# Kernel tuning notes

Hardware: AMD Instinct MI355X
Metric: run time of the kernel (lower is better)

The kernel has to match this reference:

```python
import jax, jax.numpy as jnp
import numpy as np

N = 1_000_000   # gaussians
K_NB = 10       # neighbor control points per gaussian
K_TOTAL = 300   # num_fine control points


def _normalize(q, eps=1e-8):
    return q / jnp.maximum(jnp.linalg.norm(q, axis=-1, keepdims=True), eps)


def quaternion_to_rotation_matrix(q):
    # q: [..., 4] in (w, x, y, z); normalized before conversion
    q = _normalize(q)
    w, x, y, z = q[..., 0], q[..., 1], q[..., 2], q[..., 3]
    R = jnp.stack([
        jnp.stack([1 - 2 * (y * y + z * z), 2 * (x * y - w * z), 2 * (x * z + w * y)], axis=-1),
        jnp.stack([2 * (x * y + w * z), 1 - 2 * (x * x + z * z), 2 * (y * z - w * x)], axis=-1),
        jnp.stack([2 * (x * z - w * y), 2 * (y * z + w * x), 1 - 2 * (x * x + y * y)], axis=-1),
    ], axis=-2)  # [..., 3, 3]
    return R


def quaternion_multiply(a, b):
    # Hamilton product, (w, x, y, z)
    aw, ax, ay, az = a[..., 0], a[..., 1], a[..., 2], a[..., 3]
    bw, bx, by, bz = b[..., 0], b[..., 1], b[..., 2], b[..., 3]
    return jnp.stack([
        aw * bw - ax * bx - ay * by - az * bz,
        aw * bx + ax * bw + ay * bz - az * by,
        aw * by - ax * bz + ay * bw + az * bx,
        aw * bz + ax * by - ay * bx + az * bw,
    ], axis=-1)


def setup_inputs() -> dict:
    key = jax.random.key(0)
    ks = jax.random.split(key, 7)
    means = jax.random.normal(ks[0], (N, 3), dtype=jnp.float32)
    quaternions = _normalize(jax.random.normal(ks[1], (N, 4), dtype=jnp.float32))
    w = jax.random.uniform(ks[2], (N, K_NB), dtype=jnp.float32) + 1e-3
    weights = w / w.sum(-1, keepdims=True)  # blending weights sum to 1
    indices = jax.random.randint(ks[3], (N, K_NB), 0, K_TOTAL)
    ctrl_translations = 0.1 * jax.random.normal(ks[4], (K_TOTAL, 3), dtype=jnp.float32)
    ctrl_rotations = _normalize(jax.random.normal(ks[5], (K_TOTAL, 4), dtype=jnp.float32))
    ctrl_positions = jax.random.normal(ks[6], (K_TOTAL, 3), dtype=jnp.float32)
    return {
        'means': means, 'quaternions': quaternions, 'weights': weights,
        'ctrl_translations': ctrl_translations, 'ctrl_rotations': ctrl_rotations,
        'ctrl_positions': ctrl_positions, 'indices': indices,
    }


def reference(means, quaternions, weights, ctrl_translations, ctrl_rotations, ctrl_positions, indices):
    # gather neighbor control-point transforms
    nb_trans = ctrl_translations[indices]   # [N, K, 3]
    nb_rots = ctrl_rotations[indices]       # [N, K, 4]
    nb_pos = ctrl_positions[indices]        # [N, K, 3]

    diff = means[:, None, :] - nb_pos                       # [N, K, 3]
    R_ctrl = quaternion_to_rotation_matrix(nb_rots)         # [N, K, 3, 3]
    rotated_diff = jnp.einsum('nkij,nkj->nki', R_ctrl, diff)
    deformed_per_cp = rotated_diff + nb_pos + nb_trans      # [N, K, 3]

    w = weights[..., None]                                  # [N, K, 1]
    deformed_means = (w * deformed_per_cp).sum(axis=1)      # [N, 3]

    blended_rot = _normalize((w * nb_rots).sum(axis=1))     # [N, 4]
    deformed_quats = quaternion_multiply(blended_rot, quaternions)
    return deformed_means, deformed_quats
```

## Files before the change

kernel.cpp:

```cpp
#include <hip/hip_runtime.h>
#include <math.h>


__device__ __forceinline__ void compute_cp(
    const float* __restrict__ ctrl_trans,
    const float* __restrict__ ctrl_rot,
    const float* __restrict__ ctrl_pos,
    int cp, float4* q_out, float4* b_out)
{
    float qw = ctrl_rot[cp * 4 + 0];
    float qx = ctrl_rot[cp * 4 + 1];
    float qy = ctrl_rot[cp * 4 + 2];
    float qz = ctrl_rot[cp * 4 + 3];
    float n   = sqrtf(qw * qw + qx * qx + qy * qy + qz * qz);
    float inv = 1.0f / fmaxf(n, 1e-8f);
    float w = qw * inv, x = qx * inv, y = qy * inv, z = qz * inv;
    float R00 = 1.0f - 2.0f * (y * y + z * z);
    float R01 = 2.0f * (x * y - w * z);
    float R02 = 2.0f * (x * z + w * y);
    float R10 = 2.0f * (x * y + w * z);
    float R11 = 1.0f - 2.0f * (x * x + z * z);
    float R12 = 2.0f * (y * z - w * x);
    float R20 = 2.0f * (x * z - w * y);
    float R21 = 2.0f * (y * z + w * x);
    float R22 = 1.0f - 2.0f * (x * x + y * y);
    float px = ctrl_pos[cp * 3 + 0];
    float py = ctrl_pos[cp * 3 + 1];
    float pz = ctrl_pos[cp * 3 + 2];
    float tx = ctrl_trans[cp * 3 + 0];
    float ty = ctrl_trans[cp * 3 + 1];
    float tz = ctrl_trans[cp * 3 + 2];
    *q_out = make_float4(w, x, y, z);
    *b_out = make_float4(px + tx - (R00 * px + R01 * py + R02 * pz),
                         py + ty - (R10 * px + R11 * py + R12 * pz),
                         pz + tz - (R20 * px + R21 * py + R22 * pz),
                         0.0f);
}

struct Accum {
    float W;
    float Mxx, Myy, Mzz, Mxy, Mxz, Myz, Mwx, Mwy, Mwz;
    float qsw, qsx, qsy, qsz;
    float bsx, bsy, bsz;
};

__device__ __forceinline__ void acc_init(Accum& a) {
    a.W = 0.0f;
    a.Mxx = a.Myy = a.Mzz = 0.0f;
    a.Mxy = a.Mxz = a.Myz = 0.0f;
    a.Mwx = a.Mwy = a.Mwz = 0.0f;
    a.qsw = a.qsx = a.qsy = a.qsz = 0.0f;
    a.bsx = a.bsy = a.bsz = 0.0f;
}

__device__ __forceinline__ void acc_neighbor(Accum& a, const float4* __restrict__ s4,
                                             int cp, float w) {
    float4 q = s4[2 * cp];
    float4 b = s4[2 * cp + 1];
    float tw = w * q.x, tx = w * q.y, ty = w * q.z, tz = w * q.w;
    a.W += w;
    a.Mxx = fmaf(tx, q.y, a.Mxx);
    a.Myy = fmaf(ty, q.z, a.Myy);
    a.Mzz = fmaf(tz, q.w, a.Mzz);
    a.Mxy = fmaf(tx, q.z, a.Mxy);
    a.Mxz = fmaf(tx, q.w, a.Mxz);
    a.Myz = fmaf(ty, q.w, a.Myz);
    a.Mwx = fmaf(tw, q.y, a.Mwx);
    a.Mwy = fmaf(tw, q.z, a.Mwy);
    a.Mwz = fmaf(tw, q.w, a.Mwz);
    a.qsw += tw; a.qsx += tx; a.qsy += ty; a.qsz += tz;
    a.bsx = fmaf(w, b.x, a.bsx);
    a.bsy = fmaf(w, b.y, a.bsy);
    a.bsz = fmaf(w, b.z, a.bsz);
}

__device__ __forceinline__ void acc_epilogue(const Accum& a,
                                             float mx, float my, float mz,
                                             float4 g,
                                             float* dmx, float* dmy, float* dmz,
                                             float4* oq) {
    float A00 = a.W - 2.0f * (a.Myy + a.Mzz);
    float A01 = 2.0f * (a.Mxy - a.Mwz);
    float A02 = 2.0f * (a.Mxz + a.Mwy);
    float A10 = 2.0f * (a.Mxy + a.Mwz);
    float A11 = a.W - 2.0f * (a.Mxx + a.Mzz);
    float A12 = 2.0f * (a.Myz - a.Mwx);
    float A20 = 2.0f * (a.Mxz - a.Mwy);
    float A21 = 2.0f * (a.Myz + a.Mwx);
    float A22 = a.W - 2.0f * (a.Mxx + a.Myy);

    *dmx = fmaf(A00, mx, fmaf(A01, my, fmaf(A02, mz, a.bsx)));
    *dmy = fmaf(A10, mx, fmaf(A11, my, fmaf(A12, mz, a.bsy)));
    *dmz = fmaf(A20, mx, fmaf(A21, my, fmaf(A22, mz, a.bsz)));

    float n   = sqrtf(a.qsw * a.qsw + a.qsx * a.qsx + a.qsy * a.qsy + a.qsz * a.qsz);
    float inv = 1.0f / fmaxf(n, 1e-8f);
    float bw = a.qsw * inv, bx = a.qsx * inv, by = a.qsy * inv, bz = a.qsz * inv;

    float gw = g.x, gx = g.y, gy = g.z, gz = g.w;
    oq->x = bw * gw - bx * gx - by * gy - bz * gz;
    oq->y = bw * gx + bx * gw + by * gz - bz * gy;
    oq->z = bw * gy - bx * gz + by * gw + bz * gx;
    oq->w = bw * gz + bx * gy - by * gx + bz * gw;
}

__global__ __launch_bounds__(256) void deform_pair_kernel(
    const float* __restrict__ means,
    const float* __restrict__ quats,
    const float* __restrict__ weights,
    const float* __restrict__ ctrl_trans,
    const float* __restrict__ ctrl_rot,
    const float* __restrict__ ctrl_pos,
    const int*   __restrict__ indices,
    float* __restrict__ out_means,
    float* __restrict__ out_quats,
    int N, int K_TOTAL)
{
    extern __shared__ float4 s4[];
    for (int cp = threadIdx.x; cp < K_TOTAL; cp += blockDim.x) {
        float4 q, b;
        compute_cp(ctrl_trans, ctrl_rot, ctrl_pos, cp, &q, &b);
        s4[2 * cp]     = q;
        s4[2 * cp + 1] = b;
    }
    __syncthreads();

    long long tid = (long long)blockIdx.x * blockDim.x + threadIdx.x;
    long long i0  = 2 * tid;
    if (i0 >= N) return;

    if (i0 + 1 < N) {
        const int4*   ip = (const int4*)(indices + i0 * 10);
        const float4* wp = (const float4*)(weights + i0 * 10);
        int4   I0 = ip[0], I1 = ip[1], I2 = ip[2], I3 = ip[3], I4 = ip[4];
        float4 W0 = wp[0], W1 = wp[1], W2 = wp[2], W3 = wp[3], W4 = wp[4];

        Accum a0; acc_init(a0);
        acc_neighbor(a0, s4, I0.x, W0.x);
        acc_neighbor(a0, s4, I0.y, W0.y);
        acc_neighbor(a0, s4, I0.z, W0.z);
        acc_neighbor(a0, s4, I0.w, W0.w);
        acc_neighbor(a0, s4, I1.x, W1.x);
        acc_neighbor(a0, s4, I1.y, W1.y);
        acc_neighbor(a0, s4, I1.z, W1.z);
        acc_neighbor(a0, s4, I1.w, W1.w);
        acc_neighbor(a0, s4, I2.x, W2.x);
        acc_neighbor(a0, s4, I2.y, W2.y);

        Accum a1; acc_init(a1);
        acc_neighbor(a1, s4, I2.z, W2.z);
        acc_neighbor(a1, s4, I2.w, W2.w);
        acc_neighbor(a1, s4, I3.x, W3.x);
        acc_neighbor(a1, s4, I3.y, W3.y);
        acc_neighbor(a1, s4, I3.z, W3.z);
        acc_neighbor(a1, s4, I3.w, W3.w);
        acc_neighbor(a1, s4, I4.x, W4.x);
        acc_neighbor(a1, s4, I4.y, W4.y);
        acc_neighbor(a1, s4, I4.z, W4.z);
        acc_neighbor(a1, s4, I4.w, W4.w);

        const float2* mp = (const float2*)(means + i0 * 3);
        float2 m01 = mp[0], m23 = mp[1], m45 = mp[2];

        float4 g0 = ((const float4*)quats)[i0];
        float4 g1 = ((const float4*)quats)[i0 + 1];

        float d0x, d0y, d0z, d1x, d1y, d1z;
        float4 oq0, oq1;
        acc_epilogue(a0, m01.x, m01.y, m23.x, g0, &d0x, &d0y, &d0z, &oq0);
        acc_epilogue(a1, m23.y, m45.x, m45.y, g1, &d1x, &d1y, &d1z, &oq1);

        float2* omp = (float2*)(out_means + i0 * 3);
        omp[0] = make_float2(d0x, d0y);
        omp[1] = make_float2(d0z, d1x);
        omp[2] = make_float2(d1y, d1z);

        float4* oqp = (float4*)(out_quats + i0 * 4);
        oqp[0] = oq0;
        oqp[1] = oq1;
    } else {
        const int*   idx_row = indices + i0 * 10;
        const float* w_row   = weights + i0 * 10;
        Accum a0; acc_init(a0);
#pragma unroll
        for (int k = 0; k < 10; k++)
            acc_neighbor(a0, s4, idx_row[k], w_row[k]);

        float mx = means[i0 * 3 + 0];
        float my = means[i0 * 3 + 1];
        float mz = means[i0 * 3 + 2];
        float4 g0 = ((const float4*)quats)[i0];
        float dx, dy, dz;
        float4 oq0;
        acc_epilogue(a0, mx, my, mz, g0, &dx, &dy, &dz, &oq0);
        out_means[i0 * 3 + 0] = dx;
        out_means[i0 * 3 + 1] = dy;
        out_means[i0 * 3 + 2] = dz;
        ((float4*)out_quats)[i0] = oq0;
    }
}

__global__ __launch_bounds__(256) void deform_generic_kernel(
    const float* __restrict__ means,
    const float* __restrict__ quats,
    const float* __restrict__ weights,
    const float* __restrict__ ctrl_trans,
    const float* __restrict__ ctrl_rot,
    const float* __restrict__ ctrl_pos,
    const int*   __restrict__ indices,
    float* __restrict__ out_means,
    float* __restrict__ out_quats,
    int N, int K_NB, int K_TOTAL)
{
    extern __shared__ float4 s4[];
    for (int cp = threadIdx.x; cp < K_TOTAL; cp += blockDim.x) {
        float4 q, b;
        compute_cp(ctrl_trans, ctrl_rot, ctrl_pos, cp, &q, &b);
        s4[2 * cp]     = q;
        s4[2 * cp + 1] = b;
    }
    __syncthreads();

    long long i = (long long)blockIdx.x * blockDim.x + threadIdx.x;
    if (i >= N) return;

    const int*   idx_row = indices + i * K_NB;
    const float* w_row   = weights + i * K_NB;
    Accum a0; acc_init(a0);
    for (int k = 0; k < K_NB; k++)
        acc_neighbor(a0, s4, idx_row[k], w_row[k]);

    float mx = means[i * 3 + 0];
    float my = means[i * 3 + 1];
    float mz = means[i * 3 + 2];
    float4 g0 = ((const float4*)quats)[i];
    float dx, dy, dz;
    float4 oq0;
    acc_epilogue(a0, mx, my, mz, g0, &dx, &dy, &dz, &oq0);
    out_means[i * 3 + 0] = dx;
    out_means[i * 3 + 1] = dy;
    out_means[i * 3 + 2] = dz;
    ((float4*)out_quats)[i] = oq0;
}

extern "C" void kernel_launch(void* const* d_in, const int* in_sizes, int n_in,
                              void* d_out, int out_size, void* d_ws, size_t ws_size,
                              hipStream_t stream) {
    const float* means      = (const float*)d_in[0];
    const float* quats      = (const float*)d_in[1];
    const float* weights    = (const float*)d_in[2];
    const float* ctrl_trans = (const float*)d_in[3];
    const float* ctrl_rot   = (const float*)d_in[4];
    const float* ctrl_pos   = (const float*)d_in[5];
    const int*   indices    = (const int*)d_in[6];

    int N       = in_sizes[0] / 3;
    int K_NB    = in_sizes[2] / N;
    int K_TOTAL = in_sizes[3] / 3;

    float* out_means = (float*)d_out;
    float* out_quats = (float*)d_out + (long long)N * 3;

    int block = 256;
    size_t smem = (size_t)K_TOTAL * 2 * sizeof(float4);

    if (K_NB == 10) {
        long long pairs = ((long long)N + 1) / 2;
        int grid = (int)((pairs + block - 1) / block);
        deform_pair_kernel<<<grid, block, smem, stream>>>(
            means, quats, weights, ctrl_trans, ctrl_rot, ctrl_pos, indices,
            out_means, out_quats, N, K_TOTAL);
    } else {
        int grid = (int)(((long long)N + block - 1) / block);
        deform_generic_kernel<<<grid, block, smem, stream>>>(
            means, quats, weights, ctrl_trans, ctrl_rot, ctrl_pos, indices,
            out_means, out_quats, N, K_NB, K_TOTAL);
    }
}
```

Before: 149.4 us.

## Use grid-stride persistent blocks and split shared control-point table into SoA

The pair kernel now launches at most 1536 blocks that loop over pairs with a grid stride. Each block therefore builds the control-point table in shared memory once and reuses it for many pairs, instead of every one of roughly 2000 blocks recomputing it. The shared table moves from interleaved (q, b) pairs to two separate arrays, which changes the LDS bank access pattern. Loads of means and quats are also hoisted ahead of the accumulation, and ctrl_rot is read as a single float4. The risk is that fewer resident blocks per CU reduce the memory-level parallelism available to hide latency.

```diff
diff --git a/kernel.cpp b/kernel.cpp
--- a/kernel.cpp
+++ b/kernel.cpp
@@ -8,10 +8,8 @@
     const float* __restrict__ ctrl_pos,
     int cp, float4* q_out, float4* b_out)
 {
-    float qw = ctrl_rot[cp * 4 + 0];
-    float qx = ctrl_rot[cp * 4 + 1];
-    float qy = ctrl_rot[cp * 4 + 2];
-    float qz = ctrl_rot[cp * 4 + 3];
+    float4 qv = ((const float4*)ctrl_rot)[cp];
+    float qw = qv.x, qx = qv.y, qy = qv.z, qz = qv.w;
     float n   = sqrtf(qw * qw + qx * qx + qy * qy + qz * qz);
     float inv = 1.0f / fmaxf(n, 1e-8f);
     float w = qw * inv, x = qx * inv, y = qy * inv, z = qz * inv;
@@ -54,9 +52,9 @@
 }
 
 __device__ __forceinline__ void acc_neighbor(Accum& a, const float4* __restrict__ s4,
-                                             int cp, float w) {
-    float4 q = s4[2 * cp];
-    float4 b = s4[2 * cp + 1];
+                                             int K_TOTAL, int cp, float w) {
+    float4 q = s4[cp];
+    float4 b = s4[K_TOTAL + cp];
     float tw = w * q.x, tx = w * q.y, ty = w * q.z, tz = w * q.w;
     a.W += w;
     a.Mxx = fmaf(tx, q.y, a.Mxx);
@@ -114,89 +112,89 @@
     const int*   __restrict__ indices,
     float* __restrict__ out_means,
     float* __restrict__ out_quats,
-    int N, int K_TOTAL)
+    int N, int K_TOTAL, long long n_pairs)
 {
     extern __shared__ float4 s4[];
     for (int cp = threadIdx.x; cp < K_TOTAL; cp += blockDim.x) {
         float4 q, b;
         compute_cp(ctrl_trans, ctrl_rot, ctrl_pos, cp, &q, &b);
-        s4[2 * cp]     = q;
-        s4[2 * cp + 1] = b;
+        s4[cp]           = q;
+        s4[K_TOTAL + cp] = b;
     }
     __syncthreads();
 
-    long long tid = (long long)blockIdx.x * blockDim.x + threadIdx.x;
-    long long i0  = 2 * tid;
-    if (i0 >= N) return;
-
-    if (i0 + 1 < N) {
-        const int4*   ip = (const int4*)(indices + i0 * 10);
-        const float4* wp = (const float4*)(weights + i0 * 10);
-        int4   I0 = ip[0], I1 = ip[1], I2 = ip[2], I3 = ip[3], I4 = ip[4];
-        float4 W0 = wp[0], W1 = wp[1], W2 = wp[2], W3 = wp[3], W4 = wp[4];
-
-        Accum a0; acc_init(a0);
-        acc_neighbor(a0, s4, I0.x, W0.x);
-        acc_neighbor(a0, s4, I0.y, W0.y);
-        acc_neighbor(a0, s4, I0.z, W0.z);
-        acc_neighbor(a0, s4, I0.w, W0.w);
-        acc_neighbor(a0, s4, I1.x, W1.x);
-        acc_neighbor(a0, s4, I1.y, W1.y);
-        acc_neighbor(a0, s4, I1.z, W1.z);
-        acc_neighbor(a0, s4, I1.w, W1.w);
-        acc_neighbor(a0, s4, I2.x, W2.x);
-        acc_neighbor(a0, s4, I2.y, W2.y);
-
-        Accum a1; acc_init(a1);
-        acc_neighbor(a1, s4, I2.z, W2.z);
-        acc_neighbor(a1, s4, I2.w, W2.w);
-        acc_neighbor(a1, s4, I3.x, W3.x);
-        acc_neighbor(a1, s4, I3.y, W3.y);
-        acc_neighbor(a1, s4, I3.z, W3.z);
-        acc_neighbor(a1, s4, I3.w, W3.w);
-        acc_neighbor(a1, s4, I4.x, W4.x);
-        acc_neighbor(a1, s4, I4.y, W4.y);
-        acc_neighbor(a1, s4, I4.z, W4.z);
-        acc_neighbor(a1, s4, I4.w, W4.w);
-
-        const float2* mp = (const float2*)(means + i0 * 3);
-        float2 m01 = mp[0], m23 = mp[1], m45 = mp[2];
-
-        float4 g0 = ((const float4*)quats)[i0];
-        float4 g1 = ((const float4*)quats)[i0 + 1];
-
-        float d0x, d0y, d0z, d1x, d1y, d1z;
-        float4 oq0, oq1;
-        acc_epilogue(a0, m01.x, m01.y, m23.x, g0, &d0x, &d0y, &d0z, &oq0);
-        acc_epilogue(a1, m23.y, m45.x, m45.y, g1, &d1x, &d1y, &d1z, &oq1);
-
-        float2* omp = (float2*)(out_means + i0 * 3);
-        omp[0] = make_float2(d0x, d0y);
-        omp[1] = make_float2(d0z, d1x);
-        omp[2] = make_float2(d1y, d1z);
-
-        float4* oqp = (float4*)(out_quats + i0 * 4);
-        oqp[0] = oq0;
-        oqp[1] = oq1;
-    } else {
-        const int*   idx_row = indices + i0 * 10;
-        const float* w_row   = weights + i0 * 10;
-        Accum a0; acc_init(a0);
+    long long stride = (long long)gridDim.x * blockDim.x;
+    for (long long p = (long long)blockIdx.x * blockDim.x + threadIdx.x;
+         p < n_pairs; p += stride) {
+        long long i0 = 2 * p;
+
+        if (i0 + 1 < N) {
+            const int4*   ip = (const int4*)(indices + i0 * 10);
+            const float4* wp = (const float4*)(weights + i0 * 10);
+            int4   I0 = ip[0], I1 = ip[1], I2 = ip[2], I3 = ip[3], I4 = ip[4];
+            float4 W0 = wp[0], W1 = wp[1], W2 = wp[2], W3 = wp[3], W4 = wp[4];
+            const float2* mp = (const float2*)(means + i0 * 3);
+            float2 m01 = mp[0], m23 = mp[1], m45 = mp[2];
+            float4 g0 = ((const float4*)quats)[i0];
+            float4 g1 = ((const float4*)quats)[i0 + 1];
+
+            Accum a0; acc_init(a0);
+            acc_neighbor(a0, s4, K_TOTAL, I0.x, W0.x);
+            acc_neighbor(a0, s4, K_TOTAL, I0.y, W0.y);
+            acc_neighbor(a0, s4, K_TOTAL, I0.z, W0.z);
+            acc_neighbor(a0, s4, K_TOTAL, I0.w, W0.w);
+            acc_neighbor(a0, s4, K_TOTAL, I1.x, W1.x);
+            acc_neighbor(a0, s4, K_TOTAL, I1.y, W1.y);
+            acc_neighbor(a0, s4, K_TOTAL, I1.z, W1.z);
+            acc_neighbor(a0, s4, K_TOTAL, I1.w, W1.w);
+            acc_neighbor(a0, s4, K_TOTAL, I2.x, W2.x);
+            acc_neighbor(a0, s4, K_TOTAL, I2.y, W2.y);
+
+            Accum a1; acc_init(a1);
+            acc_neighbor(a1, s4, K_TOTAL, I2.z, W2.z);
+            acc_neighbor(a1, s4, K_TOTAL, I2.w, W2.w);
+            acc_neighbor(a1, s4, K_TOTAL, I3.x, W3.x);
+            acc_neighbor(a1, s4, K_TOTAL, I3.y, W3.y);
+            acc_neighbor(a1, s4, K_TOTAL, I3.z, W3.z);
+            acc_neighbor(a1, s4, K_TOTAL, I3.w, W3.w);
+            acc_neighbor(a1, s4, K_TOTAL, I4.x, W4.x);
+            acc_neighbor(a1, s4, K_TOTAL, I4.y, W4.y);
+            acc_neighbor(a1, s4, K_TOTAL, I4.z, W4.z);
+            acc_neighbor(a1, s4, K_TOTAL, I4.w, W4.w);
+
+            float d0x, d0y, d0z, d1x, d1y, d1z;
+            float4 oq0, oq1;
+            acc_epilogue(a0, m01.x, m01.y, m23.x, g0, &d0x, &d0y, &d0z, &oq0);
+            acc_epilogue(a1, m23.y, m45.x, m45.y, g1, &d1x, &d1y, &d1z, &oq1);
+
+            float2* omp = (float2*)(out_means + i0 * 3);
+            omp[0] = make_float2(d0x, d0y);
+            omp[1] = make_float2(d0z, d1x);
+            omp[2] = make_float2(d1y, d1z);
+
+            float4* oqp = (float4*)(out_quats + i0 * 4);
+            oqp[0] = oq0;
+            oqp[1] = oq1;
+        } else {
+            const int*   idx_row = indices + i0 * 10;
+            const float* w_row   = weights + i0 * 10;
+            Accum a0; acc_init(a0);
 #pragma unroll
-        for (int k = 0; k < 10; k++)
-            acc_neighbor(a0, s4, idx_row[k], w_row[k]);
-
-        float mx = means[i0 * 3 + 0];
-        float my = means[i0 * 3 + 1];
-        float mz = means[i0 * 3 + 2];
-        float4 g0 = ((const float4*)quats)[i0];
-        float dx, dy, dz;
-        float4 oq0;
-        acc_epilogue(a0, mx, my, mz, g0, &dx, &dy, &dz, &oq0);
-        out_means[i0 * 3 + 0] = dx;
-        out_means[i0 * 3 + 1] = dy;
-        out_means[i0 * 3 + 2] = dz;
-        ((float4*)out_quats)[i0] = oq0;
+            for (int k = 0; k < 10; k++)
+                acc_neighbor(a0, s4, K_TOTAL, idx_row[k], w_row[k]);
+
+            float mx = means[i0 * 3 + 0];
+            float my = means[i0 * 3 + 1];
+            float mz = means[i0 * 3 + 2];
+            float4 g0 = ((const float4*)quats)[i0];
+            float dx, dy, dz;
+            float4 oq0;
+            acc_epilogue(a0, mx, my, mz, g0, &dx, &dy, &dz, &oq0);
+            out_means[i0 * 3 + 0] = dx;
+            out_means[i0 * 3 + 1] = dy;
+            out_means[i0 * 3 + 2] = dz;
+            ((float4*)out_quats)[i0] = oq0;
+        }
     }
 }
 
@@ -216,8 +214,8 @@
     for (int cp = threadIdx.x; cp < K_TOTAL; cp += blockDim.x) {
         float4 q, b;
         compute_cp(ctrl_trans, ctrl_rot, ctrl_pos, cp, &q, &b);
-        s4[2 * cp]     = q;
-        s4[2 * cp + 1] = b;
+        s4[cp]           = q;
+        s4[K_TOTAL + cp] = b;
     }
     __syncthreads();
 
@@ -228,7 +226,7 @@
     const float* w_row   = weights + i * K_NB;
     Accum a0; acc_init(a0);
     for (int k = 0; k < K_NB; k++)
-        acc_neighbor(a0, s4, idx_row[k], w_row[k]);
+        acc_neighbor(a0, s4, K_TOTAL, idx_row[k], w_row[k]);
 
     float mx = means[i * 3 + 0];
     float my = means[i * 3 + 1];
@@ -265,11 +263,12 @@
     size_t smem = (size_t)K_TOTAL * 2 * sizeof(float4);
 
     if (K_NB == 10) {
-        long long pairs = ((long long)N + 1) / 2;
-        int grid = (int)((pairs + block - 1) / block);
+        long long n_pairs = ((long long)N + 1) / 2;
+        long long blocks  = (n_pairs + block - 1) / block;
+        int grid = (int)(blocks < 1536 ? blocks : 1536);
         deform_pair_kernel<<<grid, block, smem, stream>>>(
             means, quats, weights, ctrl_trans, ctrl_rot, ctrl_pos, indices,
-            out_means, out_quats, N, K_TOTAL);
+            out_means, out_quats, N, K_TOTAL, n_pairs);
     } else {
         int grid = (int)(((long long)N + block - 1) / block);
         deform_generic_kernel<<<grid, block, smem, stream>>>(
```

Result: no change. 152.2 us (+1.9%).
